# Kernel tuning notes

Measured on AMD Instinct MI355X. Metric: run time of the kernel, lower is better.

## Reference

```python
import jax, jax.numpy as jnp
import numpy as np

HIDDEN = 128
NUM_HEADS = 8
F32_MIN = jnp.finfo(jnp.float32).min


def _split_heads(x, n):
    # [B, S, D] -> [B, n, S, D//n]
    b, s, d = x.shape
    return x.reshape(b, s, n, d // n).transpose(0, 2, 1, 3)


def setup_inputs() -> dict:
    key = jax.random.key(0)
    k1, k2, k3 = jax.random.split(key, 3)
    B, S = 4, 2048
    key_and_value = jax.random.normal(k1, (B, S, 2 * HIDDEN), dtype=jnp.float32)
    query = jax.random.normal(k2, (B, S, HIDDEN), dtype=jnp.float32)
    seq_len = jax.random.randint(k3, (B, 1), 1, S + 1, dtype=jnp.int32)
    return {"key_and_value": key_and_value, "query": query, "seq_len": seq_len}


def reference(key_and_value, query, seq_len):
    B, S, _ = query.shape
    d_head = HIDDEN // NUM_HEADS
    k, v = jnp.split(key_and_value, 2, axis=2)           # each [B, S, HIDDEN]
    Q = _split_heads(query, NUM_HEADS) * (d_head ** 0.5)  # NOTE: original MULTIPLIES by sqrt(d_head)
    K = _split_heads(k, NUM_HEADS)
    V = _split_heads(v, NUM_HEADS)
    # scores: [B, H, S, S]
    logits = jnp.einsum('bhqd,bhkd->bhqk', Q, K)
    # length mask over key positions: valid where pos < seq_len (one-hot+cumsum trick)
    valid = (jnp.arange(S, dtype=jnp.int32)[None, :] < seq_len).astype(jnp.float32)  # [B, S]
    logits = logits + F32_MIN * (1.0 - valid[:, None, None, :])
    weights = jax.nn.softmax(logits, axis=-1)
    out = jnp.einsum('bhqk,bhkd->bhqd', weights, V)       # [B, H, S, d_head]
    return out.transpose(0, 2, 1, 3).reshape(B, S, HIDDEN)
```

## Files before the change

kernel.cpp:

```cpp
#include <hip/hip_runtime.h>
#include <hip/hip_bf16.h>

#define HIDDEN 128
#define NHEAD  8
#define DHEAD  16
#define KBLK   64
#define QBLK   64
#define CHUNK  512
#define TILEB  6144
#define QSCALE 5.77078016355585277626f

typedef __attribute__((ext_vector_type(8))) __bf16 bf16x8;
typedef __attribute__((ext_vector_type(4))) __bf16 bf16x4;
typedef __attribute__((ext_vector_type(4))) float  f32x4;
typedef __attribute__((ext_vector_type(2))) float  f32x2;
typedef __attribute__((ext_vector_type(4))) int    i32x4;

__device__ __forceinline__ int ksub(int k)  { return ((k >> 5) << 1) | ((k >> 2) & 1); }
__device__ __forceinline__ int kirow(int k) { return (((k >> 3) & 3) << 2) | (k & 3); }


__device__ __forceinline__ void cvt_store(char* Sb, int ka, i32x4 vaddr,
                                          f32x4 kvec, f32x4 vvec)
{
    bf16x4 khv, klv;
    #pragma unroll
    for (int i = 0; i < 4; ++i) {
        __bf16 hi = (__bf16)kvec[i];
        khv[i] = hi;
        klv[i] = (__bf16)(kvec[i] - (float)hi);
    }
    *(bf16x4*)(Sb + ka)        = khv;
    *(bf16x4*)(Sb + 2048 + ka) = klv;
    #pragma unroll
    for (int i = 0; i < 4; ++i)
        *(__bf16*)(Sb + vaddr[i]) = (__bf16)vvec[i];
}

template<bool SPLIT>
__global__ __launch_bounds__(256, 4)
void mha_fwd(const float* __restrict__ kv,
             const float* __restrict__ q,
             const int*   __restrict__ seq_len,
             float* __restrict__ out,
             float* __restrict__ pbuf,
             float* __restrict__ mlbuf,
             int S, int nc)
{
    const int qtile = blockIdx.x;
    const int h     = blockIdx.y;
    int b, c0;
    if (SPLIT) { b = blockIdx.z / nc; c0 = blockIdx.z % nc; }
    else       { b = blockIdx.z;      c0 = 0; }
    const int L = seq_len[b];
    const int kstart = SPLIT ? c0 * CHUNK : 0;
    if (SPLIT && kstart >= L) return;
    const int kend = SPLIT ? min(L, kstart + CHUNK) : L;

    const int tid  = threadIdx.x;
    const int lane = tid & 63;
    const int wave = tid >> 6;
    const int g    = lane >> 4;
    const int lr   = lane & 15;
    const int sw   = (lr & 7) << 4;

    __shared__ __align__(16) char Stg[2][TILEB];

    const int qbase = qtile * QBLK + wave * 16;
    bf16x8 qfrag;
    {
        const float* qp = q + ((size_t)(b * S + qbase + lr) * HIDDEN) + h * DHEAD + (g & 1) * 8;
        #pragma unroll
        for (int j = 0; j < 8; ++j) {
            float qv = qp[j] * QSCALE;
            __bf16 hi = (__bf16)qv;
            qfrag[j] = (g < 2) ? hi : (__bf16)(qv - (float)hi);
        }
    }

    const int sk = tid >> 2;
    const int qd = tid & 3;
    const float* kvp = kv + ((size_t)(b * S + sk) * (2 * HIDDEN)) + h * DHEAD + 4 * qd;
    const int ka = ksub(sk) * 512 + (qd >> 1) * 256 + kirow(sk) * 16 + (qd & 1) * 8;
    i32x4 vaddr;
    #pragma unroll
    for (int i = 0; i < 4; ++i) {
        const int d = 4 * qd + i;
        vaddr[i] = 4096 + d * 128 + (((sk >> 3) * 16) ^ ((d & 7) << 4)) + (sk & 7) * 2;
    }

    f32x4 acc = {0.f, 0.f, 0.f, 0.f};
    float m = -1e30f, lsum = 0.f;

    const int ntiles = (kend - kstart + KBLK - 1) >> 6;

    {
        const float* kp = kvp + (size_t)kstart * (2 * HIDDEN);
        f32x4 kvec = *(const f32x4*)kp;
        f32x4 vvec = *(const f32x4*)(kp + HIDDEN);
        cvt_store(&Stg[0][0], ka, vaddr, kvec, vvec);
    }
    __syncthreads();

    for (int ti = 0; ti < ntiles; ++ti) {
        const int kb = kstart + ti * KBLK;
        const char* Sb = &Stg[ti & 1][0];
        const bool hasnext = (ti + 1) < ntiles;

        f32x4 nkv, nvv;
        if (hasnext) {
            const float* kp = kvp + (size_t)(kb + KBLK) * (2 * HIDDEN);
            nkv = *(const f32x4*)kp;
            nvv = *(const f32x4*)(kp + HIDDEN);
        }

        bf16x8 kfh[4], kfl[4];
        #pragma unroll
        for (int sub = 0; sub < 4; ++sub) {
            kfh[sub] = *(const bf16x8*)(Sb + sub * 512 + (g & 1) * 256 + lr * 16);
            kfl[sub] = *(const bf16x8*)(Sb + 2048 + sub * 512 + (g & 1) * 256 + lr * 16);
        }
        bf16x8 vb0 = *(const bf16x8*)(Sb + 4096 + lr * 128 + ((g * 16) ^ sw));
        bf16x8 vb1 = *(const bf16x8*)(Sb + 4096 + lr * 128 + ((64 + g * 16) ^ sw));

        f32x4 s[4];
        #pragma unroll
        for (int sub = 0; sub < 4; ++sub) {
            f32x4 z = {0.f, 0.f, 0.f, 0.f};
            z = __builtin_amdgcn_mfma_f32_16x16x32_bf16(kfh[sub], qfrag, z, 0, 0, 0);
            s[sub] = __builtin_amdgcn_mfma_f32_16x16x32_bf16(kfl[sub], qfrag, z, 0, 0, 0);
        }
        if (kb + KBLK > kend) {
            #pragma unroll
            for (int sub = 0; sub < 4; ++sub) {
                const int kb2 = kb + (sub >> 1) * 32 + (sub & 1) * 4 + g * 8;
                #pragma unroll
                for (int r = 0; r < 4; ++r)
                    if (kb2 + r >= kend) s[sub][r] = -1e30f;
            }
        }

        float t0 = fmaxf(fmaxf(s[0][0], s[0][1]), fmaxf(s[0][2], s[0][3]));
        float t1 = fmaxf(fmaxf(s[1][0], s[1][1]), fmaxf(s[1][2], s[1][3]));
        float t2 = fmaxf(fmaxf(s[2][0], s[2][1]), fmaxf(s[2][2], s[2][3]));
        float t3 = fmaxf(fmaxf(s[3][0], s[3][1]), fmaxf(s[3][2], s[3][3]));
        float tmax = fmaxf(fmaxf(t0, t1), fmaxf(t2, t3));
        tmax = fmaxf(tmax, __shfl_xor(tmax, 16));
        tmax = fmaxf(tmax, __shfl_xor(tmax, 32));

        const float mn = fmaxf(m, tmax);
        const float alpha = exp2f(m - mn);
        m = mn;

        float rsum = 0.f;
        bf16x8 pa0, pa1;
        #pragma unroll
        for (int sub = 0; sub < 2; ++sub)
            #pragma unroll
            for (int r = 0; r < 4; ++r) {
                float p = exp2f(s[sub][r] - mn);
                rsum += p;
                pa0[sub * 4 + r] = (__bf16)p;
            }
        #pragma unroll
        for (int sub = 2; sub < 4; ++sub)
            #pragma unroll
            for (int r = 0; r < 4; ++r) {
                float p = exp2f(s[sub][r] - mn);
                rsum += p;
                pa1[(sub - 2) * 4 + r] = (__bf16)p;
            }
        rsum += __shfl_xor(rsum, 16);
        rsum += __shfl_xor(rsum, 32);
        lsum = lsum * alpha + rsum;
        acc *= alpha;

        acc = __builtin_amdgcn_mfma_f32_16x16x32_bf16(vb0, pa0, acc, 0, 0, 0);
        acc = __builtin_amdgcn_mfma_f32_16x16x32_bf16(vb1, pa1, acc, 0, 0, 0);

        if (hasnext)
            cvt_store(&Stg[(ti + 1) & 1][0], ka, vaddr, nkv, nvv);
        __syncthreads();
    }

    const int qglob = qbase + lr;
    if (SPLIT) {
        const size_t row = (((size_t)b * nc + c0) * S + qglob) * NHEAD + h;
        *(f32x4*)&pbuf[row * DHEAD + g * 4] = acc;
        if (g == 0) { f32x2 ml = {m, lsum}; *(f32x2*)&mlbuf[row * 2] = ml; }
    } else {
        const float inv = 1.0f / lsum;
        *(f32x4*)&out[((size_t)b * S + qglob) * HIDDEN + h * DHEAD + g * 4] = acc * inv;
    }
}

__global__ __launch_bounds__(256)
void mha_merge(const float* __restrict__ pbuf, const float* __restrict__ mlbuf,
               const int* __restrict__ seq_len, float* __restrict__ out, int S, int nc)
{
    const int t = blockIdx.x * 256 + threadIdx.x;
    const int h = t & (NHEAD - 1);
    const int rest = t >> 3;
    const int qg = rest % S;
    const int b  = rest / S;
    const int L  = seq_len[b];
    const int nch = (L + CHUNK - 1) / CHUNK;

    const size_t cstr = (size_t)S * NHEAD;
    const size_t row0 = ((size_t)b * nc) * cstr + (size_t)qg * NHEAD + h;

    float mv[8], lv[8];
    float M = -1e30f;
    for (int c = 0; c < nch; ++c) {
        f32x2 ml = *(const f32x2*)&mlbuf[(row0 + c * cstr) * 2];
        mv[c] = ml[0]; lv[c] = ml[1];
        M = fmaxf(M, ml[0]);
    }
    float den = 0.f;
    f32x4 o0 = {0,0,0,0}, o1 = o0, o2 = o0, o3 = o0;
    for (int c = 0; c < nch; ++c) {
        float w = exp2f(mv[c] - M);
        den += w * lv[c];
        const float* pp = &pbuf[(row0 + c * cstr) * DHEAD];
        o0 += w * *(const f32x4*)&pp[0];
        o1 += w * *(const f32x4*)&pp[4];
        o2 += w * *(const f32x4*)&pp[8];
        o3 += w * *(const f32x4*)&pp[12];
    }
    const float inv = 1.0f / den;
    float* op = &out[((size_t)b * S + qg) * HIDDEN + h * DHEAD];
    *(f32x4*)&op[0]  = o0 * inv;
    *(f32x4*)&op[4]  = o1 * inv;
    *(f32x4*)&op[8]  = o2 * inv;
    *(f32x4*)&op[12] = o3 * inv;
}

extern "C" void kernel_launch(void* const* d_in, const int* in_sizes, int n_in,
                              void* d_out, int out_size, void* d_ws, size_t ws_size,
                              hipStream_t stream)
{
    const float* kv      = (const float*)d_in[0];
    const float* query   = (const float*)d_in[1];
    const int*   seq_len = (const int*)d_in[2];
    float* out           = (float*)d_out;

    const int B = in_sizes[2];
    const int S = in_sizes[1] / (B * HIDDEN);
    const int nc = (S + CHUNK - 1) / CHUNK;

    const size_t pb  = (size_t)B * nc * S * NHEAD * DHEAD * sizeof(float);
    const size_t mlb = (size_t)B * nc * S * NHEAD * 2 * sizeof(float);

    if (nc <= 8 && ws_size >= pb + mlb) {
        float* pbuf  = (float*)d_ws;
        float* mlbuf = (float*)((char*)d_ws + pb);
        mha_fwd<true><<<dim3(S / QBLK, NHEAD, B * nc), dim3(256), 0, stream>>>(
            kv, query, seq_len, nullptr, pbuf, mlbuf, S, nc);
        const int nrows = B * S * NHEAD;
        mha_merge<<<dim3((nrows + 255) / 256), dim3(256), 0, stream>>>(pbuf, mlbuf, seq_len, out, S, nc);
    } else {
        mha_fwd<false><<<dim3(S / QBLK, NHEAD, B), dim3(256), 0, stream>>>(
            kv, query, seq_len, out, nullptr, nullptr, S, 1);
    }
}
```

Measured before the change: 45.00 us.

## Process two query tiles per block, shrink key chunk to 256, reorder grid

Each block now handles two 64-row query tiles that share every staged K/V tile. This halves the global-load and bf16-conversion cost per query row and gives each wave more independent MFMA work between barriers. Key chunks drop from 512 to 256 (up to 8 chunks) so the grid keeps roughly the same block count despite the fewer query blocks. The grid z index is now chunk-major rather than batch-major. The cost is more registers per thread (two accumulators and two q fragments), a larger partial-result buffer, and more merge work.

```diff
diff --git a/kernel.cpp b/kernel.cpp
--- a/kernel.cpp
+++ b/kernel.cpp
@@ -5,8 +5,7 @@
 #define NHEAD  8
 #define DHEAD  16
 #define KBLK   64
-#define QBLK   64
-#define CHUNK  512
+#define QPB    2
 #define TILEB  6144
 #define QSCALE 5.77078016355585277626f
 
@@ -18,7 +17,6 @@
 
 __device__ __forceinline__ int ksub(int k)  { return ((k >> 5) << 1) | ((k >> 2) & 1); }
 __device__ __forceinline__ int kirow(int k) { return (((k >> 3) & 3) << 2) | (k & 3); }
-
 
 __device__ __forceinline__ void cvt_store(char* Sb, int ka, i32x4 vaddr,
                                           f32x4 kvec, f32x4 vvec)
@@ -45,17 +43,17 @@
              float* __restrict__ out,
              float* __restrict__ pbuf,
              float* __restrict__ mlbuf,
-             int S, int nc)
-{
-    const int qtile = blockIdx.x;
+             int S, int nc, int chunk)
+{
+    const int qpair = blockIdx.x;
     const int h     = blockIdx.y;
     int b, c0;
-    if (SPLIT) { b = blockIdx.z / nc; c0 = blockIdx.z % nc; }
-    else       { b = blockIdx.z;      c0 = 0; }
+    if (SPLIT) { const int Bn = gridDim.z / nc; b = blockIdx.z % Bn; c0 = blockIdx.z / Bn; }
+    else       { b = blockIdx.z; c0 = 0; }
     const int L = seq_len[b];
-    const int kstart = SPLIT ? c0 * CHUNK : 0;
+    const int kstart = SPLIT ? c0 * chunk : 0;
     if (SPLIT && kstart >= L) return;
-    const int kend = SPLIT ? min(L, kstart + CHUNK) : L;
+    const int kend = SPLIT ? min(L, kstart + chunk) : L;
 
     const int tid  = threadIdx.x;
     const int lane = tid & 63;
@@ -66,15 +64,16 @@
 
     __shared__ __align__(16) char Stg[2][TILEB];
 
-    const int qbase = qtile * QBLK + wave * 16;
-    bf16x8 qfrag;
-    {
-        const float* qp = q + ((size_t)(b * S + qbase + lr) * HIDDEN) + h * DHEAD + (g & 1) * 8;
+    const int qrowb = qpair * (QPB * KBLK) + wave * 16 + lr;
+    bf16x8 qf[QPB];
+    #pragma unroll
+    for (int qt = 0; qt < QPB; ++qt) {
+        const float* qp = q + ((size_t)(b * S + qrowb + qt * KBLK) * HIDDEN) + h * DHEAD + (g & 1) * 8;
         #pragma unroll
         for (int j = 0; j < 8; ++j) {
             float qv = qp[j] * QSCALE;
             __bf16 hi = (__bf16)qv;
-            qfrag[j] = (g < 2) ? hi : (__bf16)(qv - (float)hi);
+            qf[qt][j] = (g < 2) ? hi : (__bf16)(qv - (float)hi);
         }
     }
 
@@ -89,8 +88,13 @@
         vaddr[i] = 4096 + d * 128 + (((sk >> 3) * 16) ^ ((d & 7) << 4)) + (sk & 7) * 2;
     }
 
-    f32x4 acc = {0.f, 0.f, 0.f, 0.f};
-    float m = -1e30f, lsum = 0.f;
+    f32x4 acc[QPB];
+    float m[QPB], lsum[QPB];
+    #pragma unroll
+    for (int qt = 0; qt < QPB; ++qt) {
+        acc[qt] = (f32x4){0.f, 0.f, 0.f, 0.f};
+        m[qt] = -1e30f; lsum[qt] = 0.f;
+    }
 
     const int ntiles = (kend - kstart + KBLK - 1) >> 6;
 
@@ -123,80 +127,89 @@
         bf16x8 vb0 = *(const bf16x8*)(Sb + 4096 + lr * 128 + ((g * 16) ^ sw));
         bf16x8 vb1 = *(const bf16x8*)(Sb + 4096 + lr * 128 + ((64 + g * 16) ^ sw));
 
-        f32x4 s[4];
+        const bool bnd = (kb + KBLK > kend);
+
         #pragma unroll
-        for (int sub = 0; sub < 4; ++sub) {
-            f32x4 z = {0.f, 0.f, 0.f, 0.f};
-            z = __builtin_amdgcn_mfma_f32_16x16x32_bf16(kfh[sub], qfrag, z, 0, 0, 0);
-            s[sub] = __builtin_amdgcn_mfma_f32_16x16x32_bf16(kfl[sub], qfrag, z, 0, 0, 0);
-        }
-        if (kb + KBLK > kend) {
+        for (int qt = 0; qt < QPB; ++qt) {
+            f32x4 s[4];
             #pragma unroll
             for (int sub = 0; sub < 4; ++sub) {
-                const int kb2 = kb + (sub >> 1) * 32 + (sub & 1) * 4 + g * 8;
+                f32x4 z = {0.f, 0.f, 0.f, 0.f};
+                z = __builtin_amdgcn_mfma_f32_16x16x32_bf16(kfh[sub], qf[qt], z, 0, 0, 0);
+                s[sub] = __builtin_amdgcn_mfma_f32_16x16x32_bf16(kfl[sub], qf[qt], z, 0, 0, 0);
+            }
+            if (bnd) {
                 #pragma unroll
-                for (int r = 0; r < 4; ++r)
-                    if (kb2 + r >= kend) s[sub][r] = -1e30f;
+                for (int sub = 0; sub < 4; ++sub) {
+                    const int kb2 = kb + (sub >> 1) * 32 + (sub & 1) * 4 + g * 8;
+                    #pragma unroll
+                    for (int r = 0; r < 4; ++r)
+                        if (kb2 + r >= kend) s[sub][r] = -1e30f;
+                }
             }
-        }
-
-        float t0 = fmaxf(fmaxf(s[0][0], s[0][1]), fmaxf(s[0][2], s[0][3]));
-        float t1 = fmaxf(fmaxf(s[1][0], s[1][1]), fmaxf(s[1][2], s[1][3]));
-        float t2 = fmaxf(fmaxf(s[2][0], s[2][1]), fmaxf(s[2][2], s[2][3]));
-        float t3 = fmaxf(fmaxf(s[3][0], s[3][1]), fmaxf(s[3][2], s[3][3]));
-        float tmax = fmaxf(fmaxf(t0, t1), fmaxf(t2, t3));
-        tmax = fmaxf(tmax, __shfl_xor(tmax, 16));
-        tmax = fmaxf(tmax, __shfl_xor(tmax, 32));
-
-        const float mn = fmaxf(m, tmax);
-        const float alpha = exp2f(m - mn);
-        m = mn;
-
-        float rsum = 0.f;
-        bf16x8 pa0, pa1;
-        #pragma unroll
-        for (int sub = 0; sub < 2; ++sub)
+
+            float t0 = fmaxf(fmaxf(s[0][0], s[0][1]), fmaxf(s[0][2], s[0][3]));
+            float t1 = fmaxf(fmaxf(s[1][0], s[1][1]), fmaxf(s[1][2], s[1][3]));
+            float t2 = fmaxf(fmaxf(s[2][0], s[2][1]), fmaxf(s[2][2], s[2][3]));
+            float t3 = fmaxf(fmaxf(s[3][0], s[3][1]), fmaxf(s[3][2], s[3][3]));
+            float tmax = fmaxf(fmaxf(t0, t1), fmaxf(t2, t3));
+            tmax = fmaxf(tmax, __shfl_xor(tmax, 16));
+            tmax = fmaxf(tmax, __shfl_xor(tmax, 32));
+
+            const float mn = fmaxf(m[qt], tmax);
+            const float alpha = exp2f(m[qt] - mn);
+            m[qt] = mn;
+
+            float rsum = 0.f;
+            bf16x8 pa0, pa1;
             #pragma unroll
-            for (int r = 0; r < 4; ++r) {
-                float p = exp2f(s[sub][r] - mn);
-                rsum += p;
-                pa0[sub * 4 + r] = (__bf16)p;
-            }
-        #pragma unroll
-        for (int sub = 2; sub < 4; ++sub)
+            for (int sub = 0; sub < 2; ++sub)
+                #pragma unroll
+                for (int r = 0; r < 4; ++r) {
+                    float p = exp2f(s[sub][r] - mn);
+                    rsum += p;
+                    pa0[sub * 4 + r] = (__bf16)p;
+                }
             #pragma unroll
-            for (int r = 0; r < 4; ++r) {
-                float p = exp2f(s[sub][r] - mn);
-                rsum += p;
-                pa1[(sub - 2) * 4 + r] = (__bf16)p;
-            }
-        rsum += __shfl_xor(rsum, 16);
-        rsum += __shfl_xor(rsum, 32);
-        lsum = lsum * alpha + rsum;
-        acc *= alpha;
-
-        acc = __builtin_amdgcn_mfma_f32_16x16x32_bf16(vb0, pa0, acc, 0, 0, 0);
-        acc = __builtin_amdgcn_mfma_f32_16x16x32_bf16(vb1, pa1, acc, 0, 0, 0);
+            for (int sub = 2; sub < 4; ++sub)
+                #pragma unroll
+                for (int r = 0; r < 4; ++r) {
+                    float p = exp2f(s[sub][r] - mn);
+                    rsum += p;
+                    pa1[(sub - 2) * 4 + r] = (__bf16)p;
+                }
+            rsum += __shfl_xor(rsum, 16);
+            rsum += __shfl_xor(rsum, 32);
+            lsum[qt] = lsum[qt] * alpha + rsum;
+            acc[qt] *= alpha;
+
+            acc[qt] = __builtin_amdgcn_mfma_f32_16x16x32_bf16(vb0, pa0, acc[qt], 0, 0, 0);
+            acc[qt] = __builtin_amdgcn_mfma_f32_16x16x32_bf16(vb1, pa1, acc[qt], 0, 0, 0);
+        }
 
         if (hasnext)
             cvt_store(&Stg[(ti + 1) & 1][0], ka, vaddr, nkv, nvv);
         __syncthreads();
     }
 
-    const int qglob = qbase + lr;
-    if (SPLIT) {
-        const size_t row = (((size_t)b * nc + c0) * S + qglob) * NHEAD + h;
-        *(f32x4*)&pbuf[row * DHEAD + g * 4] = acc;
-        if (g == 0) { f32x2 ml = {m, lsum}; *(f32x2*)&mlbuf[row * 2] = ml; }
-    } else {
-        const float inv = 1.0f / lsum;
-        *(f32x4*)&out[((size_t)b * S + qglob) * HIDDEN + h * DHEAD + g * 4] = acc * inv;
+    #pragma unroll
+    for (int qt = 0; qt < QPB; ++qt) {
+        const int qglob = qrowb + qt * KBLK;
+        if (SPLIT) {
+            const size_t row = (((size_t)b * nc + c0) * S + qglob) * NHEAD + h;
+            *(f32x4*)&pbuf[row * DHEAD + g * 4] = acc[qt];
+            if (g == 0) { f32x2 ml = {m[qt], lsum[qt]}; *(f32x2*)&mlbuf[row * 2] = ml; }
+        } else {
+            const float inv = 1.0f / lsum[qt];
+            *(f32x4*)&out[((size_t)b * S + qglob) * HIDDEN + h * DHEAD + g * 4] = acc[qt] * inv;
+        }
     }
 }
 
 __global__ __launch_bounds__(256)
 void mha_merge(const float* __restrict__ pbuf, const float* __restrict__ mlbuf,
-               const int* __restrict__ seq_len, float* __restrict__ out, int S, int nc)
+               const int* __restrict__ seq_len, float* __restrict__ out,
+               int S, int nc, int chunk)
 {
     const int t = blockIdx.x * 256 + threadIdx.x;
     const int h = t & (NHEAD - 1);
@@ -204,7 +217,7 @@
     const int qg = rest % S;
     const int b  = rest / S;
     const int L  = seq_len[b];
-    const int nch = (L + CHUNK - 1) / CHUNK;
+    const int nch = min(nc, (L + chunk - 1) / chunk);
 
     const size_t cstr = (size_t)S * NHEAD;
     const size_t row0 = ((size_t)b * nc) * cstr + (size_t)qg * NHEAD + h;
@@ -246,20 +259,26 @@
 
     const int B = in_sizes[2];
     const int S = in_sizes[1] / (B * HIDDEN);
-    const int nc = (S + CHUNK - 1) / CHUNK;
-
-    const size_t pb  = (size_t)B * nc * S * NHEAD * DHEAD * sizeof(float);
-    const size_t mlb = (size_t)B * nc * S * NHEAD * 2 * sizeof(float);
-
-    if (nc <= 8 && ws_size >= pb + mlb) {
+
+    int chunk = 0, nc = 1;
+    size_t pb = 0, mlb = 0;
+    for (int cand = 256; cand <= 512; cand <<= 1) {
+        int n = (S + cand - 1) / cand;
+        size_t pbc  = (size_t)B * n * S * NHEAD * DHEAD * sizeof(float);
+        size_t mlbc = (size_t)B * n * S * NHEAD * 2 * sizeof(float);
+        if (n <= 8 && ws_size >= pbc + mlbc) { chunk = cand; nc = n; pb = pbc; mlb = mlbc; break; }
+    }
+
+    if (chunk) {
         float* pbuf  = (float*)d_ws;
         float* mlbuf = (float*)((char*)d_ws + pb);
-        mha_fwd<true><<<dim3(S / QBLK, NHEAD, B * nc), dim3(256), 0, stream>>>(
-            kv, query, seq_len, nullptr, pbuf, mlbuf, S, nc);
+        mha_fwd<true><<<dim3(S / (QPB * KBLK), NHEAD, B * nc), dim3(256), 0, stream>>>(
+            kv, query, seq_len, nullptr, pbuf, mlbuf, S, nc, chunk);
         const int nrows = B * S * NHEAD;
-        mha_merge<<<dim3((nrows + 255) / 256), dim3(256), 0, stream>>>(pbuf, mlbuf, seq_len, out, S, nc);
+        mha_merge<<<dim3((nrows + 255) / 256), dim3(256), 0, stream>>>(
+            pbuf, mlbuf, seq_len, out, S, nc, chunk);
     } else {
-        mha_fwd<false><<<dim3(S / QBLK, NHEAD, B), dim3(256), 0, stream>>>(
-            kv, query, seq_len, out, nullptr, nullptr, S, 1);
-    }
-}
+        mha_fwd<false><<<dim3(S / (QPB * KBLK), NHEAD, B), dim3(256), 0, stream>>>(
+            kv, query, seq_len, out, nullptr, nullptr, S, 1, S);
+    }
+}
```

Result: slower. 47.27 us (+5.0%).
